# Optimization experiments

Measured on AMD Instinct MI355X. Metric: run time of the kernel, lower is better.

Reference implementation:

```python
import jax, jax.numpy as jnp
import numpy as np
from jax import lax

# IVF+PQ search (FAISS IVF1024,PQ8x8 with nprobe=32, by_residual=False variant):
# 1) coarse quantizer: L2 distance of each query to nlist centroids, keep top nprobe lists
# 2) ADC: per-query LUT of squared distances between query subvectors and PQ codebooks,
#    database distance = sum over subquantizers of LUT gathered at the stored codes
# 3) mask database vectors whose IVF list was not probed, return indices of top_k smallest

NPROBE = 32  # top_n_centroids
BIG = jnp.float32(1e30)


def setup_inputs() -> dict:
    key = jax.random.key(0)
    ks = jax.random.split(key, 5)
    Q, D = 256, 128
    M, K = 8, 256          # pq_subvecs, 2**pq_nbits
    dsub = D // M          # 16
    nlist = 1024
    N = 250_000            # database size
    queries = jax.random.normal(ks[0], (Q, D), dtype=jnp.float32)
    centroids = jax.random.normal(ks[1], (nlist, D), dtype=jnp.float32)
    codebooks = jax.random.normal(ks[2], (M, K, dsub), dtype=jnp.float32)
    db_codes = jax.random.randint(ks[3], (N, M), 0, K, dtype=jnp.int32)
    db_list = jax.random.randint(ks[4], (N,), 0, nlist, dtype=jnp.int32)
    return {"queries": queries, "centroids": centroids, "codebooks": codebooks,
            "db_codes": db_codes, "db_list": db_list, "top_k": 100}


def _masked_adc_distances(queries, centroids, codebooks, db_codes, db_list):
    Q, D = queries.shape
    nlist = centroids.shape[0]
    M, K, dsub = codebooks.shape
    # ---- coarse quantizer: ||q - c||^2 over [Q, nlist] ----
    coarse = (jnp.sum(queries * queries, -1, keepdims=True)
              + jnp.sum(centroids * centroids, -1)[None, :]
              - 2.0 * queries @ centroids.T)
    _, probed = lax.top_k(-coarse, NPROBE)                      # [Q, NPROBE] list ids
    probe_mask = jnp.zeros((Q, nlist), dtype=bool).at[
        jnp.arange(Q)[:, None], probed].set(True)               # [Q, nlist]
    allowed = probe_mask[:, db_list]                            # [Q, N]
    # ---- PQ ADC lookup table: ||q_sub - codeword||^2, [Q, M, K] ----
    qs = queries.reshape(Q, M, dsub)
    lut = (jnp.sum(qs * qs, -1)[:, :, None]
           + jnp.sum(codebooks * codebooks, -1)[None, :, :]
           - 2.0 * jnp.einsum('qmd,mkd->qmk', qs, codebooks))   # [Q, M, K]
    # ---- accumulate gathered LUT entries over subquantizers ----
    dist = lut[:, 0, db_codes[:, 0]]                            # [Q, N]
    for m in range(1, M):
        dist = dist + lut[:, m, db_codes[:, m]]
    return jnp.where(allowed, dist, BIG)


def reference(queries, centroids, codebooks, db_codes, db_list, top_k):
    dist = _masked_adc_distances(queries, centroids, codebooks, db_codes, db_list)
    _, indices = lax.top_k(-dist, top_k)                        # smallest distances
    return indices
```

## Files before the change

### kernel.cpp

```cpp
#include <hip/hip_runtime.h>

#define DDIM 128
#define MSUB 8
#define KCODE 256
#define DSUB 16
#define NLIST 1024
#define NPROBE 32
#define TOPK 100
#define HBINS 4096
#define COLL_CAP 2048
#define RCAP 10
#define SCHUNK 1024
#define STHREADS 512
#define PSTRIDE 66


__device__ __forceinline__ float xla_sumsq128(const float* x) {
  float s[16];
  #pragma unroll
  for (int j = 0; j < 16; ++j) {
    float p0 = __fmul_rn(x[j],       x[j]);
    float p1 = __fmul_rn(x[j + 16],  x[j + 16]);
    float p2 = __fmul_rn(x[j + 32],  x[j + 32]);
    float p3 = __fmul_rn(x[j + 48],  x[j + 48]);
    float p4 = __fmul_rn(x[j + 64],  x[j + 64]);
    float p5 = __fmul_rn(x[j + 80],  x[j + 80]);
    float p6 = __fmul_rn(x[j + 96],  x[j + 96]);
    float p7 = __fmul_rn(x[j + 112], x[j + 112]);
    float r0 = __fadd_rn(p0, p4);
    float r1 = __fadd_rn(p1, p5);
    float r2 = __fadd_rn(p2, p6);
    float r3 = __fadd_rn(p3, p7);
    s[j] = __fadd_rn(__fadd_rn(r0, r1), __fadd_rn(r2, r3));
  }
  float a[8], b[4], c[2];
  #pragma unroll
  for (int j = 0; j < 8; ++j) a[j] = __fadd_rn(s[j], s[j + 8]);
  #pragma unroll
  for (int j = 0; j < 4; ++j) b[j] = __fadd_rn(a[j], a[j + 4]);
  #pragma unroll
  for (int j = 0; j < 2; ++j) c[j] = __fadd_rn(b[j], b[j + 2]);
  return __fadd_rn(c[0], c[1]);
}

__device__ __forceinline__ float xla_sumsq16(const float* x) {
  float p[16];
  #pragma unroll
  for (int j = 0; j < 16; ++j) p[j] = __fmul_rn(x[j], x[j]);
  float s8[8], s4[4], s2[2];
  #pragma unroll
  for (int j = 0; j < 8; ++j) s8[j] = __fadd_rn(p[j], p[j + 8]);
  #pragma unroll
  for (int j = 0; j < 4; ++j) s4[j] = __fadd_rn(s8[j], s8[j + 4]);
  #pragma unroll
  for (int j = 0; j < 2; ++j) s2[j] = __fadd_rn(s4[j], s4[j + 2]);
  return __fadd_rn(s2[0], s2[1]);
}

__device__ __forceinline__ float chain_dot16(const float* a, const float* b) {
  float dot = 0.f;
  #pragma unroll
  for (int d = 0; d < DSUB; ++d) dot = __fmaf_rn(a[d], b[d], dot);
  return dot;
}

__device__ __forceinline__ float adc_dist(const float* lut, unsigned long long code) {
  float d = lut[(unsigned)(code & 255ULL)];
  d = __fadd_rn(d, lut[256  + (unsigned)((code >> 8)  & 255ULL)]);
  d = __fadd_rn(d, lut[512  + (unsigned)((code >> 16) & 255ULL)]);
  d = __fadd_rn(d, lut[768  + (unsigned)((code >> 24) & 255ULL)]);
  d = __fadd_rn(d, lut[1024 + (unsigned)((code >> 32) & 255ULL)]);
  d = __fadd_rn(d, lut[1280 + (unsigned)((code >> 40) & 255ULL)]);
  d = __fadd_rn(d, lut[1536 + (unsigned)((code >> 48) & 255ULL)]);
  d = __fadd_rn(d, lut[1792 + (unsigned)((code >> 56) & 255ULL)]);
  return d;
}

__device__ __forceinline__ unsigned block_scan_incl(unsigned v, volatile unsigned* wsum,
                                                    int t, int nwaves) {
  int lane = t & 63, wid = t >> 6;
  #pragma unroll
  for (int off = 1; off < 64; off <<= 1) {
    unsigned u = __shfl_up(v, off, 64);
    if (lane >= off) v += u;
  }
  if (lane == 63) wsum[wid] = v;
  __syncthreads();
  if (wid == 0 && lane < nwaves) {
    unsigned wv = wsum[lane];
    #pragma unroll
    for (int off = 1; off < 16; off <<= 1) {
      unsigned u = __shfl_up(wv, off, 64);
      if (lane >= off) wv += u;
    }
    wsum[lane] = wv;
  }
  __syncthreads();
  return v + (wid > 0 ? wsum[wid - 1] : 0u);
}

__global__ __launch_bounds__(256) void k_front(const float* __restrict__ queries,
                                               const float* __restrict__ centroids,
                                               const int* __restrict__ db_list, int N,
                                               unsigned long long* __restrict__ keys_g,
                                               unsigned* __restrict__ counts) {
  const int t = threadIdx.x;
  const int r  = blockIdx.x % 5;
  const int b5 = blockIdx.x / 5;

  if (r == 0) {
    __shared__ unsigned hist_l[NLIST];
    for (int i = t; i < NLIST; i += 256) hist_l[i] = 0;
    __syncthreads();
    for (int n = b5 * 256 + t; n < N; n += 256 * 256)
      atomicAdd(&hist_l[db_list[n]], 1u);
    __syncthreads();
    for (int i = t; i < NLIST; i += 256)
      if (hist_l[i]) atomicAdd(&counts[i], hist_l[i]);
    return;
  }

  const int cid = b5 * 4 + (r - 1);
  const int qi = cid >> 2;
  const int part = cid & 3;
  __shared__ float qs[DDIM];
  if (t < DDIM) qs[t] = queries[qi * DDIM + t];
  __syncthreads();
  const float qq = xla_sumsq128(qs);
  const int c = part * 256 + t;
  const float* cr = centroids + (size_t)c * DDIM;
  float cbuf[DDIM];
  #pragma unroll
  for (int d = 0; d < DDIM; d += 4) {
    float4 cv = *(const float4*)(cr + d);
    cbuf[d] = cv.x; cbuf[d + 1] = cv.y; cbuf[d + 2] = cv.z; cbuf[d + 3] = cv.w;
  }
  const float cc = xla_sumsq128(cbuf);
  float dot = 0.f;
  #pragma unroll
  for (int d = 0; d < DDIM; ++d) dot = __fmaf_rn(qs[d], cbuf[d], dot);
  float dist = __fsub_rn(__fadd_rn(qq, cc), __fmul_rn(2.0f, dot));
  unsigned bits = __float_as_uint(dist);
  keys_g[(size_t)qi * NLIST + c] = ((unsigned long long)bits << 32) | (unsigned)c;
}

__global__ __launch_bounds__(STHREADS) void k_prep(const float* __restrict__ queries,
                                                   const float* __restrict__ codebooks,
                                                   const unsigned long long* __restrict__ keys_g,
                                                   const int* __restrict__ db_list,
                                                   const int* __restrict__ db_codes, int N,
                                                   int Q,
                                                   const unsigned* __restrict__ counts,
                                                   unsigned* __restrict__ cursor,
                                                   int4* __restrict__ pack,
                                                   float* __restrict__ lut_g,
                                                   unsigned* __restrict__ probe_g) {
  const int t = threadIdx.x;
  const int bid = blockIdx.x;

  if (bid < Q) {
    const int qi = bid;
    __shared__ float qs[DDIM];
    __shared__ unsigned hist[HBINS];
    __shared__ unsigned long long coll[512];
    __shared__ unsigned bst[NLIST + 1];
    __shared__ unsigned pstart[NPROBE], pcum[NPROBE + 1];
    __shared__ unsigned wsum[16];
    __shared__ unsigned scnt;
    __shared__ int sT;

    if (t < DDIM) qs[t] = queries[qi * DDIM + t];
    for (int i = t; i < HBINS; i += STHREADS) hist[i] = 0;
    if (t == 0) { scnt = 0; sT = HBINS - 1; }
    const unsigned long long k0 = keys_g[(size_t)qi * NLIST + t];
    const unsigned long long k1 = keys_g[(size_t)qi * NLIST + t + STHREADS];
    {
      unsigned c0 = counts[2 * t], c1 = counts[2 * t + 1];
      unsigned s2 = c0 + c1;
      unsigned incl = block_scan_incl(s2, wsum, t, STHREADS / 64);
      bst[2 * t + 1] = incl - c1;
      bst[2 * t + 2] = incl;
      if (t == 0) bst[0] = 0;
    }
    __syncthreads();

    #pragma unroll
    for (int j = 0; j < (MSUB * KCODE) / STHREADS; ++j) {
      int idx = j * STHREADS + t;
      const float* cb = codebooks + (size_t)idx * DSUB;
      const float* qsub = qs + (idx >> 8) * DSUB;
      float cbv[DSUB], qv[DSUB];
      #pragma unroll
      for (int d = 0; d < DSUB; d += 4) {
        float4 cv = *(const float4*)(cb + d);
        cbv[d] = cv.x; cbv[d + 1] = cv.y; cbv[d + 2] = cv.z; cbv[d + 3] = cv.w;
      }
      #pragma unroll
      for (int d = 0; d < DSUB; ++d) qv[d] = qsub[d];
      const float qq16 = xla_sumsq16(qv);
      const float cc16 = xla_sumsq16(cbv);
      const float dot16 = chain_dot16(qv, cbv);
      lut_g[(size_t)qi * (MSUB * KCODE) + idx] =
          __fsub_rn(__fadd_rn(qq16, cc16), __fmul_rn(2.0f, dot16));
    }

    atomicAdd(&hist[(unsigned)(k0 >> 51)], 1u);
    atomicAdd(&hist[(unsigned)(k1 >> 51)], 1u);
    __syncthreads();
    {
      unsigned mysum = 0;
      #pragma unroll
      for (int i = 0; i < HBINS / STHREADS; ++i) mysum += hist[t * (HBINS / STHREADS) + i];
      unsigned incl = block_scan_incl(mysum, wsum, t, STHREADS / 64);
      unsigned excl = incl - mysum;
      if (excl < NPROBE && NPROBE <= incl) {
        unsigned c2 = excl;
        #pragma unroll
        for (int i = 0; i < HBINS / STHREADS; ++i) {
          unsigned h = hist[t * (HBINS / STHREADS) + i];
          if (c2 + h >= NPROBE) { sT = t * (HBINS / STHREADS) + i; break; }
          c2 += h;
        }
      }
    }
    __syncthreads();
    {
      const int T32 = sT;
      if ((int)(k0 >> 51) <= T32) {
        unsigned p = atomicAdd(&scnt, 1u);
        if (p < 512) coll[p] = k0;
      }
      if ((int)(k1 >> 51) <= T32) {
        unsigned p = atomicAdd(&scnt, 1u);
        if (p < 512) coll[p] = k1;
      }
    }
    __syncthreads();
    {
      unsigned cnt = scnt; if (cnt > 512) cnt = 512;
      for (unsigned i = t; i < cnt; i += STHREADS) {
        unsigned long long k2 = coll[i];
        unsigned r = 0;
        for (unsigned j = 0; j < cnt; ++j) r += (coll[j] < k2) ? 1u : 0u;
        if (r < NPROBE) {
          unsigned l = (unsigned)(k2 & 0xffffffffULL);
          pstart[r] = bst[l];
          pcum[r + 1] = bst[l + 1] - bst[l];
        }
      }
    }
    __syncthreads();
    if (t == 0) {
      unsigned acc = 0;
      pcum[0] = 0;
      for (int j = 1; j <= NPROBE; ++j) { acc += pcum[j]; pcum[j] = acc; }
    }
    __syncthreads();
    if (t < NPROBE)     probe_g[qi * PSTRIDE + t] = pstart[t];
    if (t < NPROBE + 1) probe_g[qi * PSTRIDE + NPROBE + t] = pcum[t];
    return;
  }

  __shared__ unsigned lhist[NLIST], lbase[NLIST], sbstart[NLIST];
  __shared__ unsigned wsum2[16];
  const int base = (bid - Q) * SCHUNK;
  {
    unsigned c0 = counts[t * 2], c1 = counts[t * 2 + 1];
    unsigned sum2 = c0 + c1;
    unsigned incl = block_scan_incl(sum2, wsum2, t, STHREADS / 64);
    unsigned excl = incl - sum2;
    sbstart[t * 2] = excl;
    sbstart[t * 2 + 1] = excl + c0;
  }
  for (int i = t; i < NLIST; i += STHREADS) lhist[i] = 0;
  __syncthreads();
  #pragma unroll
  for (int k = 0; k < SCHUNK / STHREADS; ++k) {
    int n = base + k * STHREADS + t;
    if (n < N) atomicAdd(&lhist[db_list[n]], 1u);
  }
  __syncthreads();
  for (int i = t; i < NLIST; i += STHREADS) {
    unsigned cnt = lhist[i];
    if (cnt) lbase[i] = sbstart[i] + atomicAdd(&cursor[i], cnt);
    lhist[i] = 0;
  }
  __syncthreads();
  #pragma unroll
  for (int k = 0; k < SCHUNK / STHREADS; ++k) {
    int n = base + k * STHREADS + t;
    if (n < N) {
      int l = db_list[n];
      unsigned pos = lbase[l] + atomicAdd(&lhist[l], 1u);
      const int4* cp = (const int4*)(db_codes + (size_t)n * MSUB);
      int4 c0 = cp[0], c1 = cp[1];
      unsigned lo = (unsigned)(c0.x & 255) | ((unsigned)(c0.y & 255) << 8) |
                    ((unsigned)(c0.z & 255) << 16) | ((unsigned)(c0.w & 255) << 24);
      unsigned hi = (unsigned)(c1.x & 255) | ((unsigned)(c1.y & 255) << 8) |
                    ((unsigned)(c1.z & 255) << 16) | ((unsigned)(c1.w & 255) << 24);
      pack[pos] = make_int4((int)lo, (int)hi, n, 0);
    }
  }
}

__global__ __launch_bounds__(1024, 1) void k_search(const float* __restrict__ lut_g,
                                                    const unsigned* __restrict__ probe_g,
                                                    const int4* __restrict__ pack,
                                                    int* __restrict__ out) {
  const int qi = blockIdx.x;
  const int t = threadIdx.x;
  __shared__ float lut_s[MSUB * KCODE];
  __shared__ unsigned hist[HBINS];
  __shared__ unsigned long long coll[COLL_CAP];
  __shared__ unsigned pstart[NPROBE], pcum[NPROBE + 1];
  __shared__ unsigned wsum[16];
  __shared__ unsigned scnt;
  __shared__ int sT;

  lut_s[t] = lut_g[(size_t)qi * (MSUB * KCODE) + t];
  lut_s[1024 + t] = lut_g[(size_t)qi * (MSUB * KCODE) + 1024 + t];
  for (int i = t; i < HBINS; i += 1024) hist[i] = 0;
  if (t < NPROBE)     pstart[t] = probe_g[qi * PSTRIDE + t];
  if (t < NPROBE + 1) pcum[t] = probe_g[qi * PSTRIDE + NPROBE + t];
  if (t == 0) { scnt = 0; sT = HBINS - 1; }
  __syncthreads();
  const unsigned total = pcum[NPROBE];

  unsigned long long regkey[RCAP];
  int lo = 0;
  #pragma unroll
  for (int s = 0; s < RCAP; ++s) {
    unsigned g = (unsigned)t + (unsigned)(s * 1024);
    if (g < total) {
      while (pcum[lo + 1] <= g) ++lo;
      unsigned addr = pstart[lo] + (g - pcum[lo]);
      int4 w = pack[addr];
      unsigned long long code = (unsigned)w.x | ((unsigned long long)(unsigned)w.y << 32);
      unsigned bits = __float_as_uint(adc_dist(lut_s, code));
      regkey[s] = ((unsigned long long)bits << 32) | (unsigned)w.z;
      atomicAdd(&hist[bits >> 19], 1u);
    }
  }
  for (unsigned g = (unsigned)t + RCAP * 1024; g < total; g += 1024) {
    while (pcum[lo + 1] <= g) ++lo;
    unsigned addr = pstart[lo] + (g - pcum[lo]);
    int4 w = pack[addr];
    unsigned long long code = (unsigned)w.x | ((unsigned long long)(unsigned)w.y << 32);
    unsigned bits = __float_as_uint(adc_dist(lut_s, code));
    atomicAdd(&hist[bits >> 19], 1u);
  }
  __syncthreads();

  {
    unsigned mysum = 0;
    #pragma unroll
    for (int i = 0; i < 4; ++i) mysum += hist[t * 4 + i];
    unsigned incl = block_scan_incl(mysum, wsum, t, 16);
    unsigned excl = incl - mysum;
    if (excl < TOPK && TOPK <= incl) {
      unsigned c = excl;
      #pragma unroll
      for (int i = 0; i < 4; ++i) {
        unsigned h = hist[t * 4 + i];
        if (c + h >= TOPK) { sT = t * 4 + i; break; }
        c += h;
      }
    }
  }
  __syncthreads();
  const int T = sT;

  {
    #pragma unroll
    for (int s = 0; s < RCAP; ++s) {
      unsigned g = (unsigned)t + (unsigned)(s * 1024);
      if (g < total) {
        unsigned long long k2 = regkey[s];
        if ((int)(unsigned)(k2 >> 51) <= T) {
          unsigned p = atomicAdd(&scnt, 1u);
          if (p < COLL_CAP) coll[p] = k2;
        }
      }
    }
    int lo2 = 0;
    for (unsigned g = (unsigned)t + RCAP * 1024; g < total; g += 1024) {
      while (pcum[lo2 + 1] <= g) ++lo2;
      unsigned addr = pstart[lo2] + (g - pcum[lo2]);
      int4 w = pack[addr];
      unsigned long long code = (unsigned)w.x | ((unsigned long long)(unsigned)w.y << 32);
      unsigned bits = __float_as_uint(adc_dist(lut_s, code));
      if ((int)(bits >> 19) <= T) {
        unsigned p = atomicAdd(&scnt, 1u);
        if (p < COLL_CAP) coll[p] = ((unsigned long long)bits << 32) | (unsigned)w.z;
      }
    }
  }
  __syncthreads();

  unsigned cnt = scnt;
  if (cnt > COLL_CAP) cnt = COLL_CAP;
  for (unsigned i = t; i < cnt; i += 1024) {
    unsigned long long key = coll[i];
    unsigned r = 0;
    for (unsigned j = 0; j < cnt; ++j) r += (coll[j] < key) ? 1u : 0u;
    if (r < TOPK) out[qi * TOPK + r] = (int)(key & 0xffffffffULL);
  }
}

extern "C" void kernel_launch(void* const* d_in, const int* in_sizes, int n_in,
                              void* d_out, int out_size, void* d_ws, size_t ws_size,
                              hipStream_t stream) {
  const float* queries   = (const float*)d_in[0];
  const float* centroids = (const float*)d_in[1];
  const float* codebooks = (const float*)d_in[2];
  const int*   db_codes  = (const int*)d_in[3];
  const int*   db_list   = (const int*)d_in[4];
  const int N = in_sizes[4];
  const int Q = in_sizes[0] / DDIM;
  int* out = (int*)d_out;

  char* p = (char*)d_ws;
  unsigned long long* keys_g = (unsigned long long*)p; p += (size_t)Q * NLIST * 8;
  unsigned* counts = (unsigned*)p;                  p += NLIST * 4;
  unsigned* cursor = (unsigned*)p;                  p += NLIST * 4;
  int4* pack = (int4*)p;                            p += (size_t)N * 16;
  float* lut_g = (float*)p;                         p += (size_t)Q * MSUB * KCODE * 4;
  unsigned* probe_g = (unsigned*)p;                 p += (size_t)Q * PSTRIDE * 4;

  const int nscat = (N + SCHUNK - 1) / SCHUNK;

  hipMemsetAsync(counts, 0, (size_t)NLIST * 4 * 2, stream);

  k_front<<<Q * 4 + Q, 256, 0, stream>>>(queries, centroids, db_list, N, keys_g, counts);
  k_prep<<<Q + nscat, STHREADS, 0, stream>>>(queries, codebooks, keys_g, db_list,
                                             db_codes, N, Q, counts, cursor, pack,
                                             lut_g, probe_g);
  k_search<<<Q, 1024, 0, stream>>>(lut_g, probe_g, pack, out);
}
```

Baseline: 124.1 us.

## Replace atomic cursor scatter with per-chunk histograms and prefix offsets

The front kernel's histogram blocks now each cover one fixed chunk of the database and store that chunk's per-list counts in a workspace array. Each scatter block then sums the counts of all earlier chunks to get its write offsets. This removes the scatter blocks' second local histogram pass and their global atomic cursor, and makes the packed order deterministic. In exchange, the number of chunkcnt reads grows with the square of the chunk count, since later chunks scan up to about 245 earlier histograms of 4KB each. That could add significant L2 traffic to the prep kernel.

```diff
diff --git a/kernel.cpp b/kernel.cpp
--- a/kernel.cpp
+++ b/kernel.cpp
@@ -102,21 +102,31 @@
 __global__ __launch_bounds__(256) void k_front(const float* __restrict__ queries,
                                                const float* __restrict__ centroids,
                                                const int* __restrict__ db_list, int N,
+                                               int nchunk,
                                                unsigned long long* __restrict__ keys_g,
-                                               unsigned* __restrict__ counts) {
+                                               unsigned* __restrict__ counts,
+                                               unsigned* __restrict__ chunkcnt) {
   const int t = threadIdx.x;
   const int r  = blockIdx.x % 5;
   const int b5 = blockIdx.x / 5;
 
   if (r == 0) {
+    if (b5 >= nchunk) return;
     __shared__ unsigned hist_l[NLIST];
     for (int i = t; i < NLIST; i += 256) hist_l[i] = 0;
     __syncthreads();
-    for (int n = b5 * 256 + t; n < N; n += 256 * 256)
-      atomicAdd(&hist_l[db_list[n]], 1u);
-    __syncthreads();
-    for (int i = t; i < NLIST; i += 256)
-      if (hist_l[i]) atomicAdd(&counts[i], hist_l[i]);
+    const int base = b5 * SCHUNK;
+    #pragma unroll
+    for (int k = 0; k < SCHUNK / 256; ++k) {
+      int n = base + k * 256 + t;
+      if (n < N) atomicAdd(&hist_l[db_list[n]], 1u);
+    }
+    __syncthreads();
+    for (int i = t; i < NLIST; i += 256) {
+      unsigned c = hist_l[i];
+      chunkcnt[(size_t)b5 * NLIST + i] = c;
+      if (c) atomicAdd(&counts[i], c);
+    }
     return;
   }
 
@@ -151,7 +161,7 @@
                                                    const int* __restrict__ db_codes, int N,
                                                    int Q,
                                                    const unsigned* __restrict__ counts,
-                                                   unsigned* __restrict__ cursor,
+                                                   const unsigned* __restrict__ chunkcnt,
                                                    int4* __restrict__ pack,
                                                    float* __restrict__ lut_g,
                                                    unsigned* __restrict__ probe_g) {
@@ -261,37 +271,51 @@
     return;
   }
 
-  __shared__ unsigned lhist[NLIST], lbase[NLIST], sbstart[NLIST];
+  __shared__ unsigned lbase[NLIST];
+  __shared__ unsigned lrank[NLIST];
   __shared__ unsigned wsum2[16];
-  const int base = (bid - Q) * SCHUNK;
+  const int c = bid - Q;
+  const int base = c * SCHUNK;
+
   {
-    unsigned c0 = counts[t * 2], c1 = counts[t * 2 + 1];
+    unsigned c0 = counts[2 * t], c1 = counts[2 * t + 1];
     unsigned sum2 = c0 + c1;
     unsigned incl = block_scan_incl(sum2, wsum2, t, STHREADS / 64);
-    unsigned excl = incl - sum2;
-    sbstart[t * 2] = excl;
-    sbstart[t * 2 + 1] = excl + c0;
-  }
-  for (int i = t; i < NLIST; i += STHREADS) lhist[i] = 0;
-  __syncthreads();
-  #pragma unroll
-  for (int k = 0; k < SCHUNK / STHREADS; ++k) {
-    int n = base + k * STHREADS + t;
-    if (n < N) atomicAdd(&lhist[db_list[n]], 1u);
-  }
-  __syncthreads();
-  for (int i = t; i < NLIST; i += STHREADS) {
-    unsigned cnt = lhist[i];
-    if (cnt) lbase[i] = sbstart[i] + atomicAdd(&cursor[i], cnt);
-    lhist[i] = 0;
-  }
-  __syncthreads();
+    lbase[2 * t]     = incl - sum2;
+    lbase[2 * t + 1] = incl - c1;
+  }
+  for (int i = t; i < NLIST; i += STHREADS) lrank[i] = 0;
+
+  {
+    const uint2* ck2 = (const uint2*)chunkcnt;
+    unsigned s0 = 0, s1 = 0, s2 = 0, s3 = 0;
+    unsigned u0 = 0, u1 = 0, u2 = 0, u3 = 0;
+    int cc = 0;
+    for (; cc + 4 <= c; cc += 4) {
+      uint2 v0 = ck2[(size_t)(cc + 0) * (NLIST / 2) + t];
+      uint2 v1 = ck2[(size_t)(cc + 1) * (NLIST / 2) + t];
+      uint2 v2 = ck2[(size_t)(cc + 2) * (NLIST / 2) + t];
+      uint2 v3 = ck2[(size_t)(cc + 3) * (NLIST / 2) + t];
+      s0 += v0.x; u0 += v0.y;
+      s1 += v1.x; u1 += v1.y;
+      s2 += v2.x; u2 += v2.y;
+      s3 += v3.x; u3 += v3.y;
+    }
+    for (; cc < c; ++cc) {
+      uint2 v = ck2[(size_t)cc * (NLIST / 2) + t];
+      s0 += v.x; u0 += v.y;
+    }
+    lbase[2 * t]     += s0 + s1 + s2 + s3;
+    lbase[2 * t + 1] += u0 + u1 + u2 + u3;
+  }
+  __syncthreads();
+
   #pragma unroll
   for (int k = 0; k < SCHUNK / STHREADS; ++k) {
     int n = base + k * STHREADS + t;
     if (n < N) {
       int l = db_list[n];
-      unsigned pos = lbase[l] + atomicAdd(&lhist[l], 1u);
+      unsigned pos = lbase[l] + atomicAdd(&lrank[l], 1u);
       const int4* cp = (const int4*)(db_codes + (size_t)n * MSUB);
       int4 c0 = cp[0], c1 = cp[1];
       unsigned lo = (unsigned)(c0.x & 255) | ((unsigned)(c0.y & 255) << 8) |
@@ -419,21 +443,22 @@
   const int Q = in_sizes[0] / DDIM;
   int* out = (int*)d_out;
 
+  const int nchunk = (N + SCHUNK - 1) / SCHUNK;
+
   char* p = (char*)d_ws;
   unsigned long long* keys_g = (unsigned long long*)p; p += (size_t)Q * NLIST * 8;
   unsigned* counts = (unsigned*)p;                  p += NLIST * 4;
-  unsigned* cursor = (unsigned*)p;                  p += NLIST * 4;
+  unsigned* chunkcnt = (unsigned*)p;                p += (size_t)nchunk * NLIST * 4;
   int4* pack = (int4*)p;                            p += (size_t)N * 16;
   float* lut_g = (float*)p;                         p += (size_t)Q * MSUB * KCODE * 4;
   unsigned* probe_g = (unsigned*)p;                 p += (size_t)Q * PSTRIDE * 4;
 
-  const int nscat = (N + SCHUNK - 1) / SCHUNK;
-
-  hipMemsetAsync(counts, 0, (size_t)NLIST * 4 * 2, stream);
-
-  k_front<<<Q * 4 + Q, 256, 0, stream>>>(queries, centroids, db_list, N, keys_g, counts);
-  k_prep<<<Q + nscat, STHREADS, 0, stream>>>(queries, codebooks, keys_g, db_list,
-                                             db_codes, N, Q, counts, cursor, pack,
-                                             lut_g, probe_g);
+  hipMemsetAsync(counts, 0, (size_t)NLIST * 4, stream);
+
+  k_front<<<Q * 4 + Q, 256, 0, stream>>>(queries, centroids, db_list, N, nchunk,
+                                         keys_g, counts, chunkcnt);
+  k_prep<<<Q + nchunk, STHREADS, 0, stream>>>(queries, codebooks, keys_g, db_list,
+                                              db_codes, N, Q, counts, chunkcnt, pack,
+                                              lut_g, probe_g);
   k_search<<<Q, 1024, 0, stream>>>(lut_g, probe_g, pack, out);
 }
```

Result: slower. 132.5 us (+6.8%).
